# Kernel optimization log

Measured on AMD Instinct MI355X. Metric: run time of the kernel, lower is better.

## Reference

```python
import jax, jax.numpy as jnp
import numpy as np

N_NODES = 50000
N_EDGES = 400000
D_IN, D_HID, D_OUT = 512, 512, 256


def setup_inputs() -> dict:
    key = jax.random.key(0)
    k = jax.random.split(key, 6)
    x = jax.random.normal(k[0], (N_NODES, D_IN), dtype=jnp.float32)
    edge_index = jax.random.randint(k[1], (2, N_EDGES), 0, N_NODES, dtype=jnp.int64)
    # Glorot-ish init for the two GCNConv linear layers
    W1 = jax.random.normal(k[2], (D_IN, D_HID), dtype=jnp.float32) * (1.0 / np.sqrt(D_IN))
    b1 = jnp.zeros((D_HID,), dtype=jnp.float32)
    W2 = jax.random.normal(k[3], (D_HID, D_OUT), dtype=jnp.float32) * (1.0 / np.sqrt(D_HID))
    b2 = jnp.zeros((D_OUT,), dtype=jnp.float32)
    return {"x": x, "edge_index": edge_index, "W1": W1, "b1": b1, "W2": W2, "b2": b2}


def _gcn_conv(x, W, b, src, dst, norm, n):
    """PyG GCNConv: h = x W; out[i] = sum_{j->i} norm_e * h[j] + b.
    src/dst already include self-loops; norm = d^-1/2[src] * d^-1/2[dst]."""
    h = x @ W  # [n, d_out]
    msgs = h[src] * norm[:, None]  # gather + scale per edge
    agg = jnp.zeros((n, h.shape[1]), dtype=h.dtype).at[dst].add(msgs)  # scatter-add
    return agg + b


def reference(x, edge_index, W1, b1, W2, b2):
    n = x.shape[0]
    loop = jnp.arange(n, dtype=edge_index.dtype)
    src = jnp.concatenate([edge_index[0], loop])  # add self-loops
    dst = jnp.concatenate([edge_index[1], loop])
    # symmetric normalization on the self-loop-augmented graph
    deg = jnp.zeros((n,), dtype=x.dtype).at[dst].add(1.0)
    dinv = jnp.where(deg > 0, jax.lax.rsqrt(deg), 0.0)
    norm = dinv[src] * dinv[dst]
    h = jax.nn.relu(_gcn_conv(x, W1, b1, src, dst, norm, n))
    return _gcn_conv(h, W2, b2, src, dst, norm, n)
```

## Files before the change

### kernel.cpp

```cpp
#include <hip/hip_runtime.h>
#include <stdint.h>

typedef __bf16 bf16_t;
typedef __bf16 bf16x8 __attribute__((ext_vector_type(8)));
typedef float f32x4 __attribute__((ext_vector_type(4)));

#define N_NODES  50000
#define N_EDGES  400000
#define D_IN     512
#define D_HID    512
#define D_OUTD   256
#define M_PAD    50048
#define NB_SCAN  196

__device__ __forceinline__ uint32_t f2bf_bits(float x){
    uint32_t u = __float_as_uint(x);
    return (u + 0x7fffu + ((u >> 16) & 1u)) >> 16;
}
__device__ __forceinline__ void unpack8(uint4 v, float* f){
    f[0]=__uint_as_float(v.x<<16); f[1]=__uint_as_float(v.x & 0xffff0000u);
    f[2]=__uint_as_float(v.y<<16); f[3]=__uint_as_float(v.y & 0xffff0000u);
    f[4]=__uint_as_float(v.z<<16); f[5]=__uint_as_float(v.z & 0xffff0000u);
    f[6]=__uint_as_float(v.w<<16); f[7]=__uint_as_float(v.w & 0xffff0000u);
}
__device__ __forceinline__ void glds16(const bf16_t* g, bf16_t* l){
    __builtin_amdgcn_global_load_lds(
        (const __attribute__((address_space(1))) uint32_t*)g,
        (__attribute__((address_space(3))) uint32_t*)l, 16, 0, 0);
}

__global__ __launch_bounds__(256)
void conv_x_bf16(const float* __restrict__ x, bf16_t* __restrict__ Xb){
    const int t = blockIdx.x * 256 + threadIdx.x;
    const int row = t >> 7;
    uint2 o;
    if (row < N_NODES){
        float4 v = ((const float4*)x)[t];
        o.x = f2bf_bits(v.x) | (f2bf_bits(v.y) << 16);
        o.y = f2bf_bits(v.z) | (f2bf_bits(v.w) << 16);
    } else { o.x = 0u; o.y = 0u; }
    ((uint2*)Xb)[t] = o;
}

__global__ __launch_bounds__(256)
void conv_w_both(const float* __restrict__ W1, const float* __restrict__ W2,
                 bf16_t* __restrict__ W1t, bf16_t* __restrict__ W2t){
    const int idx = blockIdx.x * 256 + threadIdx.x;
    const int n = idx >> 9;
    const int k = idx & 511;
    if (n < 512) W1t[idx] = (bf16_t)W1[k * 512 + n];
    else         W2t[(n - 512) * 512 + k] = (bf16_t)W2[k * 256 + (n - 512)];
}

__global__ __launch_bounds__(256)
void k_init_deg(int* __restrict__ deg){
    int i = blockIdx.x*256 + threadIdx.x;
    if (i < N_NODES) deg[i] = 1;
}
__global__ __launch_bounds__(256)
void k_count(const int* __restrict__ ei, int* __restrict__ deg){
    int e = blockIdx.x*256 + threadIdx.x;
    if (e < N_EDGES) atomicAdd(&deg[ei[N_EDGES + e]], 1);
}
__global__ __launch_bounds__(256)
void k_dinv(const int* __restrict__ deg, float* __restrict__ dinv){
    int i = blockIdx.x*256 + threadIdx.x;
    if (i < N_NODES) dinv[i] = rsqrtf((float)deg[i]);
}
__global__ __launch_bounds__(256)
void k_scan_block(const int* __restrict__ deg, int* __restrict__ part,
                  int* __restrict__ bsum, int n){
    __shared__ int tmp[256];
    int i = blockIdx.x*256 + threadIdx.x;
    int v = (i < n) ? (deg[i] - 1) : 0;
    tmp[threadIdx.x] = v;
    __syncthreads();
    for (int off = 1; off < 256; off <<= 1){
        int t = (threadIdx.x >= off) ? tmp[threadIdx.x - off] : 0;
        __syncthreads();
        tmp[threadIdx.x] += t;
        __syncthreads();
    }
    if (i < n) part[i] = tmp[threadIdx.x] - v;
    if (threadIdx.x == 255) bsum[blockIdx.x] = tmp[255];
}
__global__ __launch_bounds__(256)
void k_scan_bsum(const int* __restrict__ bsum, int* __restrict__ bsum2, int nb){
    __shared__ int tmp[256];
    int v = (threadIdx.x < nb) ? bsum[threadIdx.x] : 0;
    tmp[threadIdx.x] = v;
    __syncthreads();
    for (int off = 1; off < 256; off <<= 1){
        int t = (threadIdx.x >= off) ? tmp[threadIdx.x - off] : 0;
        __syncthreads();
        tmp[threadIdx.x] += t;
        __syncthreads();
    }
    if (threadIdx.x < nb) bsum2[threadIdx.x] = tmp[threadIdx.x] - v;
}
__global__ __launch_bounds__(256)
void k_finalize_rowptr(const int* __restrict__ part, const int* __restrict__ bsum2,
                       int* __restrict__ rowp, int* __restrict__ cursor, int n){
    int i = blockIdx.x*256 + threadIdx.x;
    if (i < n){ int r = part[i] + bsum2[blockIdx.x]; rowp[i] = r; cursor[i] = r; }
    if (i == 0) rowp[n] = N_EDGES;
}
__global__ __launch_bounds__(256)
void k_place(const int* __restrict__ ei, const float* __restrict__ dinv,
             int* __restrict__ cursor, int* __restrict__ csrc, float* __restrict__ cnorm){
    int e = blockIdx.x*256 + threadIdx.x;
    if (e < N_EDGES){
        int s = ei[e];
        int d = ei[N_EDGES + e];
        int p = atomicAdd(&cursor[d], 1);
        csrc[p]  = s;
        cnorm[p] = dinv[s] * dinv[d];
    }
}

__global__ __launch_bounds__(256, 2)
void gemm_bf16_mfma(const bf16_t* __restrict__ A, const bf16_t* __restrict__ Bt,
                    bf16_t* __restrict__ C, int N, int K)
{
    __shared__ bf16_t As[128*32];
    __shared__ bf16_t Bs[128*32];

    const int tid  = threadIdx.x;
    const int wave = tid >> 6;
    const int lane = tid & 63;
    const int wr = wave >> 1;
    const int wc = wave & 1;
    const int mBase = blockIdx.x * 128;
    const int nBase = blockIdx.y * 128;

    const int srow = lane >> 2;
    const int scol = (lane & 3) << 3;
    const bf16_t* Ag0 = A  + (size_t)(mBase + wave*16 + srow) * K + scol;
    const bf16_t* Ag1 = Ag0 + (size_t)64 * K;
    const bf16_t* Bg0 = Bt + (size_t)(nBase + wave*16 + srow) * K + scol;
    const bf16_t* Bg1 = Bg0 + (size_t)64 * K;
    bf16_t* As0 = &As[wave*512];
    bf16_t* As1 = &As[wave*512 + 64*32];
    bf16_t* Bs0 = &Bs[wave*512];
    bf16_t* Bs1 = &Bs[wave*512 + 64*32];

    const int m16 = lane & 15;
    const int q   = lane >> 4;
    const bf16_t* aP = &As[(wr*64 + m16)*32 + q*8];
    const bf16_t* bP = &Bs[(wc*64 + m16)*32 + q*8];

    f32x4 acc[4][4] = {};

    for (int k0 = 0; k0 < K; k0 += 32){
        glds16(Ag0 + k0, As0);
        glds16(Ag1 + k0, As1);
        glds16(Bg0 + k0, Bs0);
        glds16(Bg1 + k0, Bs1);
        __syncthreads();
        bf16x8 a[4], b[4];
        #pragma unroll
        for (int t = 0; t < 4; ++t){
            a[t] = *(const bf16x8*)(aP + t*16*32);
            b[t] = *(const bf16x8*)(bP + t*16*32);
        }
        #pragma unroll
        for (int i = 0; i < 4; ++i){
            #pragma unroll
            for (int j = 0; j < 4; ++j){
                acc[i][j] = __builtin_amdgcn_mfma_f32_16x16x32_bf16(a[i], b[j], acc[i][j], 0, 0, 0);
            }
        }
        __syncthreads();
    }

    #pragma unroll
    for (int i = 0; i < 4; ++i){
        const int row0 = mBase + wr*64 + i*16 + q*4;
        #pragma unroll
        for (int j = 0; j < 4; ++j){
            const int col = nBase + wc*64 + j*16 + m16;
            bf16_t* Cp = C + (size_t)row0 * N + col;
            #pragma unroll
            for (int r = 0; r < 4; ++r)
                Cp[(size_t)r * N] = (bf16_t)acc[i][j][r];
        }
    }
}

__global__ __launch_bounds__(256)
void agg_bias_relu_512(const bf16_t* __restrict__ T, const int* __restrict__ rowp,
                       const int* __restrict__ csrc, const float* __restrict__ cnorm,
                       const float* __restrict__ dinv, const float* __restrict__ bias,
                       bf16_t* __restrict__ H)
{
    const int gw   = (blockIdx.x * 256 + threadIdx.x) >> 6;
    const int lane = threadIdx.x & 63;
    if (gw >= N_NODES) return;
    const float di = dinv[gw];
    float acc[8];
    {
        uint4 v = ((const uint4*)(T + (size_t)gw * 512))[lane];
        float f[8]; unpack8(v, f);
        const float w = di * di;
        #pragma unroll
        for (int j = 0; j < 8; ++j) acc[j] = w * f[j];
    }
    int e = rowp[gw];
    const int e1 = rowp[gw + 1];
    for (; e + 4 <= e1; e += 4){
        const int   s0 = csrc[e],   s1 = csrc[e+1], s2 = csrc[e+2], s3 = csrc[e+3];
        const float w0 = cnorm[e],  w1 = cnorm[e+1], w2 = cnorm[e+2], w3 = cnorm[e+3];
        uint4 v0 = ((const uint4*)(T + (size_t)s0 * 512))[lane];
        uint4 v1 = ((const uint4*)(T + (size_t)s1 * 512))[lane];
        uint4 v2 = ((const uint4*)(T + (size_t)s2 * 512))[lane];
        uint4 v3 = ((const uint4*)(T + (size_t)s3 * 512))[lane];
        float f[8];
        unpack8(v0, f);
        #pragma unroll
        for (int j = 0; j < 8; ++j) acc[j] += w0 * f[j];
        unpack8(v1, f);
        #pragma unroll
        for (int j = 0; j < 8; ++j) acc[j] += w1 * f[j];
        unpack8(v2, f);
        #pragma unroll
        for (int j = 0; j < 8; ++j) acc[j] += w2 * f[j];
        unpack8(v3, f);
        #pragma unroll
        for (int j = 0; j < 8; ++j) acc[j] += w3 * f[j];
    }
    for (; e < e1; ++e){
        const int   s = csrc[e];
        const float w = cnorm[e];
        uint4 v = ((const uint4*)(T + (size_t)s * 512))[lane];
        float f[8]; unpack8(v, f);
        #pragma unroll
        for (int j = 0; j < 8; ++j) acc[j] += w * f[j];
    }
    const float4 b0 = ((const float4*)bias)[lane*2];
    const float4 b1 = ((const float4*)bias)[lane*2 + 1];
    float r[8] = {acc[0]+b0.x, acc[1]+b0.y, acc[2]+b0.z, acc[3]+b0.w,
                  acc[4]+b1.x, acc[5]+b1.y, acc[6]+b1.z, acc[7]+b1.w};
    uint4 o;
    o.x = f2bf_bits(fmaxf(r[0],0.f)) | (f2bf_bits(fmaxf(r[1],0.f)) << 16);
    o.y = f2bf_bits(fmaxf(r[2],0.f)) | (f2bf_bits(fmaxf(r[3],0.f)) << 16);
    o.z = f2bf_bits(fmaxf(r[4],0.f)) | (f2bf_bits(fmaxf(r[5],0.f)) << 16);
    o.w = f2bf_bits(fmaxf(r[6],0.f)) | (f2bf_bits(fmaxf(r[7],0.f)) << 16);
    ((uint4*)(H + (size_t)gw * 512))[lane] = o;
}

__global__ __launch_bounds__(256)
void agg_bias_out_256(const bf16_t* __restrict__ T, const int* __restrict__ rowp,
                      const int* __restrict__ csrc, const float* __restrict__ cnorm,
                      const float* __restrict__ dinv, const float* __restrict__ bias,
                      float* __restrict__ out)
{
    const int wid  = (blockIdx.x * 256 + threadIdx.x) >> 6;
    const int half = (threadIdx.x >> 5) & 1;
    const int l32  = threadIdx.x & 31;
    const int node = wid * 2 + half;
    if (node >= N_NODES) return;
    const float di = dinv[node];
    float acc[8];
    {
        uint4 v = ((const uint4*)(T + (size_t)node * 256))[l32];
        float f[8]; unpack8(v, f);
        const float w = di * di;
        #pragma unroll
        for (int j = 0; j < 8; ++j) acc[j] = w * f[j];
    }
    int e = rowp[node];
    const int e1 = rowp[node + 1];
    for (; e + 4 <= e1; e += 4){
        const int   s0 = csrc[e],   s1 = csrc[e+1], s2 = csrc[e+2], s3 = csrc[e+3];
        const float w0 = cnorm[e],  w1 = cnorm[e+1], w2 = cnorm[e+2], w3 = cnorm[e+3];
        uint4 v0 = ((const uint4*)(T + (size_t)s0 * 256))[l32];
        uint4 v1 = ((const uint4*)(T + (size_t)s1 * 256))[l32];
        uint4 v2 = ((const uint4*)(T + (size_t)s2 * 256))[l32];
        uint4 v3 = ((const uint4*)(T + (size_t)s3 * 256))[l32];
        float f[8];
        unpack8(v0, f);
        #pragma unroll
        for (int j = 0; j < 8; ++j) acc[j] += w0 * f[j];
        unpack8(v1, f);
        #pragma unroll
        for (int j = 0; j < 8; ++j) acc[j] += w1 * f[j];
        unpack8(v2, f);
        #pragma unroll
        for (int j = 0; j < 8; ++j) acc[j] += w2 * f[j];
        unpack8(v3, f);
        #pragma unroll
        for (int j = 0; j < 8; ++j) acc[j] += w3 * f[j];
    }
    for (; e < e1; ++e){
        const int   s = csrc[e];
        const float w = cnorm[e];
        uint4 v = ((const uint4*)(T + (size_t)s * 256))[l32];
        float f[8]; unpack8(v, f);
        #pragma unroll
        for (int j = 0; j < 8; ++j) acc[j] += w * f[j];
    }
    const float4 b0 = ((const float4*)bias)[l32*2];
    const float4 b1 = ((const float4*)bias)[l32*2 + 1];
    float4 o0 = {acc[0]+b0.x, acc[1]+b0.y, acc[2]+b0.z, acc[3]+b0.w};
    float4 o1 = {acc[4]+b1.x, acc[5]+b1.y, acc[6]+b1.z, acc[7]+b1.w};
    ((float4*)(out + (size_t)node * 256))[l32*2]     = o0;
    ((float4*)(out + (size_t)node * 256))[l32*2 + 1] = o1;
}

extern "C" void kernel_launch(void* const* d_in, const int* in_sizes, int n_in,
                              void* d_out, int out_size, void* d_ws, size_t ws_size,
                              hipStream_t stream)
{
    const float* x  = (const float*)d_in[0];
    const int*   ei = (const int*)d_in[1];
    const float* W1 = (const float*)d_in[2];
    const float* b1 = (const float*)d_in[3];
    const float* W2 = (const float*)d_in[4];
    const float* b2 = (const float*)d_in[5];
    float* out = (float*)d_out;

    char* w = (char*)d_ws;
    auto alloc = [&](size_t bytes) -> char* {
        char* p = w; w += (bytes + 255) & ~(size_t)255; return p;
    };
    bf16_t* Xb    = (bf16_t*)alloc((size_t)M_PAD * 512 * 2);
    bf16_t* T     = (bf16_t*)alloc((size_t)M_PAD * 512 * 2);
    bf16_t* W1t   = (bf16_t*)alloc(512 * 512 * 2);
    bf16_t* W2t   = (bf16_t*)alloc(256 * 512 * 2);
    int*    deg   = (int*)  alloc(N_NODES * 4);
    float*  dinv  = (float*)alloc(N_NODES * 4);
    int*    rowp  = (int*)  alloc((N_NODES + 1) * 4);
    int*    cursor= (int*)  alloc(N_NODES * 4);
    int*    part  = (int*)  alloc(N_NODES * 4);
    int*    bsum  = (int*)  alloc(NB_SCAN * 4);
    int*    bsum2 = (int*)  alloc(NB_SCAN * 4);
    int*    csrc  = (int*)  alloc(N_EDGES * 4);
    float*  cnorm = (float*)alloc(N_EDGES * 4);

    conv_x_bf16<<<(M_PAD*128)/256, 256, 0, stream>>>(x, Xb);
    conv_w_both<<<(768*512)/256, 256, 0, stream>>>(W1, W2, W1t, W2t);

    k_init_deg<<<NB_SCAN, 256, 0, stream>>>(deg);
    k_count   <<<(N_EDGES+255)/256, 256, 0, stream>>>(ei, deg);
    k_dinv    <<<NB_SCAN, 256, 0, stream>>>(deg, dinv);
    k_scan_block<<<NB_SCAN, 256, 0, stream>>>(deg, part, bsum, N_NODES);
    k_scan_bsum <<<1, 256, 0, stream>>>(bsum, bsum2, NB_SCAN);
    k_finalize_rowptr<<<NB_SCAN, 256, 0, stream>>>(part, bsum2, rowp, cursor, N_NODES);
    k_place   <<<(N_EDGES+255)/256, 256, 0, stream>>>(ei, dinv, cursor, csrc, cnorm);

    gemm_bf16_mfma<<<dim3(M_PAD/128, 512/128), 256, 0, stream>>>(Xb, W1t, T, 512, 512);
    agg_bias_relu_512<<<(N_NODES+3)/4, 256, 0, stream>>>(T, rowp, csrc, cnorm, dinv, b1, Xb);

    gemm_bf16_mfma<<<dim3(M_PAD/128, 256/128), 256, 0, stream>>>(Xb, W2t, T, 256, 512);
    agg_bias_out_256<<<(25000+3)/4, 256, 0, stream>>>(T, rowp, csrc, cnorm, dinv, b2, out);
}
```

Measured before the change: 401.6 us.

## Fuse degree init/count/dinv into conversion and scan kernels, add nontemporal IO

Folds degree initialization into the x-to-bf16 conversion kernel, the edge-degree atomic count into the weight conversion kernel, and the rsqrt dinv into the block scan, removing three launches. The input read and the aggregation output writes become nontemporal loads and stores. The scalar remainder loop in both aggregation kernels is replaced by one predicated three-edge block that issues its gathers together. Risks include atomics contending with the conversion work, and redundant masked loads in the tail.

```diff
diff --git a/kernel.cpp b/kernel.cpp
--- a/kernel.cpp
+++ b/kernel.cpp
@@ -4,6 +4,7 @@
 typedef __bf16 bf16_t;
 typedef __bf16 bf16x8 __attribute__((ext_vector_type(8)));
 typedef float f32x4 __attribute__((ext_vector_type(4)));
+typedef uint32_t u32x4 __attribute__((ext_vector_type(4)));
 
 #define N_NODES  50000
 #define N_EDGES  400000
@@ -30,12 +31,14 @@
 }
 
 __global__ __launch_bounds__(256)
-void conv_x_bf16(const float* __restrict__ x, bf16_t* __restrict__ Xb){
+void conv_x_bf16(const float* __restrict__ x, bf16_t* __restrict__ Xb,
+                 int* __restrict__ deg){
     const int t = blockIdx.x * 256 + threadIdx.x;
+    if (t < N_NODES) deg[t] = 1;
     const int row = t >> 7;
     uint2 o;
     if (row < N_NODES){
-        float4 v = ((const float4*)x)[t];
+        f32x4 v = __builtin_nontemporal_load(((const f32x4*)x) + t);
         o.x = f2bf_bits(v.x) | (f2bf_bits(v.y) << 16);
         o.y = f2bf_bits(v.z) | (f2bf_bits(v.w) << 16);
     } else { o.x = 0u; o.y = 0u; }
@@ -44,35 +47,24 @@
 
 __global__ __launch_bounds__(256)
 void conv_w_both(const float* __restrict__ W1, const float* __restrict__ W2,
-                 bf16_t* __restrict__ W1t, bf16_t* __restrict__ W2t){
+                 bf16_t* __restrict__ W1t, bf16_t* __restrict__ W2t,
+                 const int* __restrict__ ei, int* __restrict__ deg){
     const int idx = blockIdx.x * 256 + threadIdx.x;
+    if (idx < N_EDGES) atomicAdd(&deg[ei[N_EDGES + idx]], 1);
     const int n = idx >> 9;
     const int k = idx & 511;
     if (n < 512) W1t[idx] = (bf16_t)W1[k * 512 + n];
-    else         W2t[(n - 512) * 512 + k] = (bf16_t)W2[k * 256 + (n - 512)];
-}
-
-__global__ __launch_bounds__(256)
-void k_init_deg(int* __restrict__ deg){
-    int i = blockIdx.x*256 + threadIdx.x;
-    if (i < N_NODES) deg[i] = 1;
-}
-__global__ __launch_bounds__(256)
-void k_count(const int* __restrict__ ei, int* __restrict__ deg){
-    int e = blockIdx.x*256 + threadIdx.x;
-    if (e < N_EDGES) atomicAdd(&deg[ei[N_EDGES + e]], 1);
-}
-__global__ __launch_bounds__(256)
-void k_dinv(const int* __restrict__ deg, float* __restrict__ dinv){
-    int i = blockIdx.x*256 + threadIdx.x;
-    if (i < N_NODES) dinv[i] = rsqrtf((float)deg[i]);
-}
-__global__ __launch_bounds__(256)
-void k_scan_block(const int* __restrict__ deg, int* __restrict__ part,
-                  int* __restrict__ bsum, int n){
+    else if (n < 768) W2t[(n - 512) * 512 + k] = (bf16_t)W2[k * 256 + (n - 512)];
+}
+
+__global__ __launch_bounds__(256)
+void k_scan_dinv(const int* __restrict__ deg, float* __restrict__ dinv,
+                 int* __restrict__ part, int* __restrict__ bsum, int n){
     __shared__ int tmp[256];
     int i = blockIdx.x*256 + threadIdx.x;
-    int v = (i < n) ? (deg[i] - 1) : 0;
+    int d = (i < n) ? deg[i] : 1;
+    if (i < n) dinv[i] = rsqrtf((float)d);
+    int v = (i < n) ? (d - 1) : 0;
     tmp[threadIdx.x] = v;
     __syncthreads();
     for (int off = 1; off < 256; off <<= 1){
@@ -228,24 +220,39 @@
         #pragma unroll
         for (int j = 0; j < 8; ++j) acc[j] += w3 * f[j];
     }
-    for (; e < e1; ++e){
-        const int   s = csrc[e];
-        const float w = cnorm[e];
-        uint4 v = ((const uint4*)(T + (size_t)s * 512))[lane];
-        float f[8]; unpack8(v, f);
-        #pragma unroll
-        for (int j = 0; j < 8; ++j) acc[j] += w * f[j];
+    if (e < e1){
+        const int   s0 = csrc[e];
+        const float w0 = cnorm[e];
+        const int   i1 = (e + 1 < e1) ? e + 1 : e;
+        const int   i2 = (e + 2 < e1) ? e + 2 : e;
+        const int   s1 = csrc[i1];
+        const int   s2 = csrc[i2];
+        const float w1 = (e + 1 < e1) ? cnorm[i1] : 0.f;
+        const float w2 = (e + 2 < e1) ? cnorm[i2] : 0.f;
+        uint4 v0 = ((const uint4*)(T + (size_t)s0 * 512))[lane];
+        uint4 v1 = ((const uint4*)(T + (size_t)s1 * 512))[lane];
+        uint4 v2 = ((const uint4*)(T + (size_t)s2 * 512))[lane];
+        float f[8];
+        unpack8(v0, f);
+        #pragma unroll
+        for (int j = 0; j < 8; ++j) acc[j] += w0 * f[j];
+        unpack8(v1, f);
+        #pragma unroll
+        for (int j = 0; j < 8; ++j) acc[j] += w1 * f[j];
+        unpack8(v2, f);
+        #pragma unroll
+        for (int j = 0; j < 8; ++j) acc[j] += w2 * f[j];
     }
     const float4 b0 = ((const float4*)bias)[lane*2];
     const float4 b1 = ((const float4*)bias)[lane*2 + 1];
     float r[8] = {acc[0]+b0.x, acc[1]+b0.y, acc[2]+b0.z, acc[3]+b0.w,
                   acc[4]+b1.x, acc[5]+b1.y, acc[6]+b1.z, acc[7]+b1.w};
-    uint4 o;
+    u32x4 o;
     o.x = f2bf_bits(fmaxf(r[0],0.f)) | (f2bf_bits(fmaxf(r[1],0.f)) << 16);
     o.y = f2bf_bits(fmaxf(r[2],0.f)) | (f2bf_bits(fmaxf(r[3],0.f)) << 16);
     o.z = f2bf_bits(fmaxf(r[4],0.f)) | (f2bf_bits(fmaxf(r[5],0.f)) << 16);
     o.w = f2bf_bits(fmaxf(r[6],0.f)) | (f2bf_bits(fmaxf(r[7],0.f)) << 16);
-    ((uint4*)(H + (size_t)gw * 512))[lane] = o;
+    __builtin_nontemporal_store(o, ((u32x4*)(H + (size_t)gw * 512)) + lane);
 }
 
 __global__ __launch_bounds__(256)
@@ -291,20 +298,35 @@
         #pragma unroll
         for (int j = 0; j < 8; ++j) acc[j] += w3 * f[j];
     }
-    for (; e < e1; ++e){
-        const int   s = csrc[e];
-        const float w = cnorm[e];
-        uint4 v = ((const uint4*)(T + (size_t)s * 256))[l32];
-        float f[8]; unpack8(v, f);
-        #pragma unroll
-        for (int j = 0; j < 8; ++j) acc[j] += w * f[j];
+    if (e < e1){
+        const int   s0 = csrc[e];
+        const float w0 = cnorm[e];
+        const int   i1 = (e + 1 < e1) ? e + 1 : e;
+        const int   i2 = (e + 2 < e1) ? e + 2 : e;
+        const int   s1 = csrc[i1];
+        const int   s2 = csrc[i2];
+        const float w1 = (e + 1 < e1) ? cnorm[i1] : 0.f;
+        const float w2 = (e + 2 < e1) ? cnorm[i2] : 0.f;
+        uint4 v0 = ((const uint4*)(T + (size_t)s0 * 256))[l32];
+        uint4 v1 = ((const uint4*)(T + (size_t)s1 * 256))[l32];
+        uint4 v2 = ((const uint4*)(T + (size_t)s2 * 256))[l32];
+        float f[8];
+        unpack8(v0, f);
+        #pragma unroll
+        for (int j = 0; j < 8; ++j) acc[j] += w0 * f[j];
+        unpack8(v1, f);
+        #pragma unroll
+        for (int j = 0; j < 8; ++j) acc[j] += w1 * f[j];
+        unpack8(v2, f);
+        #pragma unroll
+        for (int j = 0; j < 8; ++j) acc[j] += w2 * f[j];
     }
     const float4 b0 = ((const float4*)bias)[l32*2];
     const float4 b1 = ((const float4*)bias)[l32*2 + 1];
-    float4 o0 = {acc[0]+b0.x, acc[1]+b0.y, acc[2]+b0.z, acc[3]+b0.w};
-    float4 o1 = {acc[4]+b1.x, acc[5]+b1.y, acc[6]+b1.z, acc[7]+b1.w};
-    ((float4*)(out + (size_t)node * 256))[l32*2]     = o0;
-    ((float4*)(out + (size_t)node * 256))[l32*2 + 1] = o1;
+    f32x4 o0 = {acc[0]+b0.x, acc[1]+b0.y, acc[2]+b0.z, acc[3]+b0.w};
+    f32x4 o1 = {acc[4]+b1.x, acc[5]+b1.y, acc[6]+b1.z, acc[7]+b1.w};
+    __builtin_nontemporal_store(o0, ((f32x4*)(out + (size_t)node * 256)) + l32*2);
+    __builtin_nontemporal_store(o1, ((f32x4*)(out + (size_t)node * 256)) + l32*2 + 1);
 }
 
 extern "C" void kernel_launch(void* const* d_in, const int* in_sizes, int n_in,
@@ -337,13 +359,10 @@
     int*    csrc  = (int*)  alloc(N_EDGES * 4);
     float*  cnorm = (float*)alloc(N_EDGES * 4);
 
-    conv_x_bf16<<<(M_PAD*128)/256, 256, 0, stream>>>(x, Xb);
-    conv_w_both<<<(768*512)/256, 256, 0, stream>>>(W1, W2, W1t, W2t);
-
-    k_init_deg<<<NB_SCAN, 256, 0, stream>>>(deg);
-    k_count   <<<(N_EDGES+255)/256, 256, 0, stream>>>(ei, deg);
-    k_dinv    <<<NB_SCAN, 256, 0, stream>>>(deg, dinv);
-    k_scan_block<<<NB_SCAN, 256, 0, stream>>>(deg, part, bsum, N_NODES);
+    conv_x_bf16<<<(M_PAD*128)/256, 256, 0, stream>>>(x, Xb, deg);
+    conv_w_both<<<1568, 256, 0, stream>>>(W1, W2, W1t, W2t, ei, deg);
+
+    k_scan_dinv<<<NB_SCAN, 256, 0, stream>>>(deg, dinv, part, bsum, N_NODES);
     k_scan_bsum <<<1, 256, 0, stream>>>(bsum, bsum2, NB_SCAN);
     k_finalize_rowptr<<<NB_SCAN, 256, 0, stream>>>(part, bsum2, rowp, cursor, N_NODES);
     k_place   <<<(N_EDGES+255)/256, 256, 0, stream>>>(ei, dinv, cursor, csrc, cnorm);
```

New measurement: 396.4 us. About the same (-1.3%).
